# Kernel optimization log

Hardware: AMD Instinct MI355X
Metric: run time of the kernel (lower is better)

The kernel has to match this reference:

```python
import jax, jax.numpy as jnp
import numpy as np

N_NODES = 100000
N_EDGES = 3200000
N_GRAPHS = 512
IN_DIM = 29   # NUM_COMPONENT_TYPES(15) + NUM_PARAMS(14)
HID = 128
LAT = 256


def setup_inputs() -> dict:
    key = jax.random.key(0)
    ks = jax.random.split(key, 16)
    x = jax.random.normal(ks[0], (N_NODES, IN_DIM), dtype=jnp.float32)
    edge_index = jax.random.randint(ks[1], (2, N_EDGES), 0, N_NODES, dtype=jnp.int64)
    batch = jnp.sort(jax.random.randint(ks[2], (N_NODES,), 0, N_GRAPHS, dtype=jnp.int64))

    def lin(k, fan_in, fan_out):
        kw, kb = jax.random.split(k)
        s = 1.0 / np.sqrt(fan_in)
        W = jax.random.uniform(kw, (fan_in, fan_out), minval=-s, maxval=s, dtype=jnp.float32)
        b = jax.random.uniform(kb, (fan_out,), minval=-s, maxval=s, dtype=jnp.float32)
        return W, b

    W1, b1 = lin(ks[3], IN_DIM, HID)
    W2, b2 = lin(ks[4], HID, HID)
    W3, b3 = lin(ks[5], HID, HID)
    Wmu, bmu = lin(ks[6], HID, LAT)
    Wlv, blv = lin(ks[7], HID, LAT)
    return {"x": x, "edge_index": edge_index, "batch": batch,
            "W1": W1, "b1": b1, "W2": W2, "b2": b2, "W3": W3, "b3": b3,
            "Wmu": Wmu, "bmu": bmu, "Wlv": Wlv, "blv": blv}


def _gcn_conv(h, W, b, src, dst, dis):
    # PyG GCNConv: out = D^-1/2 (A + I) D^-1/2 (h W) + b
    hw = h @ W                                   # [N, out]
    norm = dis[src] * dis[dst]                   # [E]
    agg = jax.ops.segment_sum(hw[src] * norm[:, None], dst, num_segments=h.shape[0])
    return agg + hw * (dis * dis)[:, None] + b   # self-loop term has norm dis[i]^2


def reference(x, edge_index, batch, W1, b1, W2, b2, W3, b3, Wmu, bmu, Wlv, blv):
    src, dst = edge_index[0], edge_index[1]
    # symmetric degree with self-loops (computed once, identical across layers)
    deg = jax.ops.segment_sum(jnp.ones(src.shape[0], jnp.float32), dst,
                              num_segments=x.shape[0]) + 1.0
    dis = jax.lax.rsqrt(deg)

    h = jax.nn.relu(_gcn_conv(x, W1, b1, src, dst, dis))
    h = jax.nn.relu(_gcn_conv(h, W2, b2, src, dst, dis))
    h = jax.nn.relu(_gcn_conv(h, W3, b3, src, dst, dis))

    # global_mean_pool over graph ids
    sums = jax.ops.segment_sum(h, batch, num_segments=N_GRAPHS)
    cnts = jax.ops.segment_sum(jnp.ones(h.shape[0], jnp.float32), batch,
                               num_segments=N_GRAPHS)
    pooled = sums / jnp.maximum(cnts, 1.0)[:, None]   # [G, HID]

    mu = pooled @ Wmu + bmu
    logvar = pooled @ Wlv + blv
    return (mu, logvar)
```

## Files before the change

kernel.cpp:

```cpp
#include <hip/hip_runtime.h>
#include <hip/hip_bf16.h>

#define N_NODES 100000
#define N_EDGES 3200000
#define N_GRAPHS 512
#define IN_DIM 29
#define HID 128
#define LAT 256
#define NB 391
#define CAP 9216

typedef unsigned int uint;
typedef unsigned short ushort;
typedef float v4f __attribute__((ext_vector_type(4)));
typedef short v8s __attribute__((ext_vector_type(8)));

__device__ __forceinline__ ushort f2bf(float f) {
    uint u = __float_as_uint(f);
    return (ushort)((u + 0x7FFFu + ((u >> 16) & 1u)) >> 16);
}
__device__ __forceinline__ float bf2f(ushort h) { return __uint_as_float(((uint)h) << 16); }
__device__ __forceinline__ float bf_lo(uint p) { return __uint_as_float(p << 16); }
__device__ __forceinline__ float bf_hi(uint p) { return __uint_as_float(p & 0xFFFF0000u); }
__device__ __forceinline__ uint pack2(float a, float b) {
    return (uint)f2bf(a) | ((uint)f2bf(b) << 16);
}

__device__ __forceinline__ void bfadd(float* a, uint4 q) {
    a[0] += bf_lo(q.x); a[1] += bf_hi(q.x);
    a[2] += bf_lo(q.y); a[3] += bf_hi(q.y);
    a[4] += bf_lo(q.z); a[5] += bf_hi(q.z);
    a[6] += bf_lo(q.w); a[7] += bf_hi(q.w);
}


__global__ __launch_bounds__(1024, 2) void k_binA(const int* __restrict__ src, const int* __restrict__ dst,
                                                  int* __restrict__ bktCnt, int* __restrict__ packed, int e) {
    __shared__ int hist[NB];
    __shared__ int base[NB];
    int t = threadIdx.x;
    for (int i = t; i < NB; i += 1024) hist[i] = 0;
    __syncthreads();
    int d[8], s[8];
    const int blockStart = blockIdx.x * 8192;
    #pragma unroll
    for (int k = 0; k < 8; ++k) {
        int idx = blockStart + k * 1024 + t;
        if (idx < e) {
            d[k] = dst[idx];
            s[k] = src[idx];
            atomicAdd(&hist[d[k] >> 8], 1);
        } else d[k] = -1;
    }
    __syncthreads();
    for (int i = t; i < NB; i += 1024) {
        int c = hist[i];
        base[i] = c ? atomicAdd(&bktCnt[i], c) : 0;
    }
    __syncthreads();
    #pragma unroll
    for (int k = 0; k < 8; ++k) {
        if (d[k] >= 0) {
            int b = d[k] >> 8;
            int pos = atomicAdd(&base[b], 1);
            if (pos < CAP) packed[b * CAP + pos] = ((d[k] & 255) << 17) | s[k];
        }
    }
}

__global__ __launch_bounds__(512) void k_bscan(const int* __restrict__ bktCnt, int* __restrict__ colStart) {
    __shared__ int sh[512];
    int t = threadIdx.x;
    int v = (t < NB) ? bktCnt[t] : 0;
    if (v > CAP) v = CAP;
    sh[t] = v;
    __syncthreads();
    for (int off = 1; off < 512; off <<= 1) {
        int x = (t >= off) ? sh[t - off] : 0;
        __syncthreads();
        sh[t] += x;
        __syncthreads();
    }
    int excl = sh[t] - v;
    if (t <= NB) colStart[t] = excl;
}

__global__ __launch_bounds__(1024, 2) void k_binB(const int* __restrict__ bktCnt, const int* __restrict__ colStart,
                                                  const int* __restrict__ packed, int* __restrict__ col,
                                                  int* __restrict__ rp, float* __restrict__ dis,
                                                  const float* __restrict__ x, float* __restrict__ xt, int n) {
    __shared__ int cnt[8192];
    __shared__ int sh[1024];
    __shared__ float sdis[256];
    const int b = blockIdx.x;
    int cntB = bktCnt[b];
    if (cntB > CAP) cntB = CAP;
    const int segS = b * CAP;
    const int colBase = colStart[b];
    int t = threadIdx.x;
    #pragma unroll
    for (int k = 0; k < 8; ++k) cnt[t + k * 1024] = 0;
    __syncthreads();
    for (int j = t; j < cntB; j += 1024) {
        int pk = packed[segS + j];
        int key = ((pk >> 17) << 5) | ((pk & 0x1FFFF) >> 12);
        atomicAdd(&cnt[key], 1);
    }
    __syncthreads();
    int base8 = t << 3;
    int v[8];
    int sum = 0;
    #pragma unroll
    for (int k = 0; k < 8; ++k) { v[k] = cnt[base8 + k]; sum += v[k]; }
    sh[t] = sum;
    __syncthreads();
    for (int off = 1; off < 1024; off <<= 1) {
        int x2 = (t >= off) ? sh[t - off] : 0;
        __syncthreads();
        sh[t] += x2;
        __syncthreads();
    }
    int run = colBase + sh[t] - sum;
    #pragma unroll
    for (int k = 0; k < 8; ++k) { cnt[base8 + k] = run; run += v[k]; }
    __syncthreads();
    if (t < 256) {
        int node = (b << 8) + t;
        int start = cnt[t << 5];
        int next = (t == 255) ? (colBase + cntB) : cnt[(t + 1) << 5];
        int deg = next - start;
        float dv = rsqrtf((float)deg + 1.0f);
        sdis[t] = dv;
        if (node <= n) rp[node] = start;
        if (node < n) dis[node] = dv;
    }
    __syncthreads();
    for (int idx = t; idx < 256 * 32; idx += 1024) {
        int loc = idx >> 5;
        int node = (b << 8) + loc;
        if (node < n) {
            int k = idx & 31;
            float vv = (k < IN_DIM) ? x[(size_t)node * IN_DIM + k] * sdis[loc] : 0.f;
            xt[((size_t)node << 5) + k] = vv;
        }
    }
    for (int j = t; j < cntB; j += 1024) {
        int pk = packed[segS + j];
        int key = ((pk >> 17) << 5) | ((pk & 0x1FFFF) >> 12);
        int pos = atomicAdd(&cnt[key], 1);
        col[pos] = pk & 0x1FFFF;
    }
}


__device__ __forceinline__ void pack_one(const float* W, ushort* hi, ushort* lo, int Ksrc, int idx) {
    int j = idx & 7;
    int lane = (idx >> 3) & 63;
    int nt = (idx >> 9) & 7;
    int ks = idx >> 12;
    int k = ks * 32 + (lane >> 4) * 8 + j;
    int n = nt * 16 + (lane & 15);
    float v = (k < Ksrc) ? W[k * 128 + n] : 0.f;
    ushort h = f2bf(v);
    ushort l = f2bf(v - bf2f(h));
    hi[idx] = h;
    lo[idx] = l;
}

__global__ __launch_bounds__(256) void k_pack_all(const float* __restrict__ W1, const float* __restrict__ W2,
                                                  const float* __restrict__ W3,
                                                  ushort* w1h, ushort* w1l, ushort* w2h, ushort* w2l,
                                                  ushort* w3h, ushort* w3l, int* __restrict__ bktCnt) {
    int idx = blockIdx.x * 256 + threadIdx.x;
    if (idx < NB) bktCnt[idx] = 0;
    if (idx < 4096) {
        pack_one(W1, w1h, w1l, IN_DIM, idx);
    } else if (idx < 4096 + 16384) {
        pack_one(W2, w2h, w2l, HID, idx - 4096);
    } else if (idx < 4096 + 32768) {
        pack_one(W3, w3h, w3l, HID, idx - 4096 - 16384);
    }
}


__global__ __launch_bounds__(256, 6) void k_agg29(const float* __restrict__ xt, const int* __restrict__ rp,
                                                  const int* __restrict__ col, const float* __restrict__ dis,
                                                  float* __restrict__ y, int n) {
    int node = (int)((blockIdx.x * 256 + threadIdx.x) >> 3);
    if (node >= n) return;
    int c4 = (threadIdx.x & 7) << 2;
    int s = rp[node], e = rp[node + 1];
    v4f A = (v4f){0.f, 0.f, 0.f, 0.f};
    v4f B = (v4f){0.f, 0.f, 0.f, 0.f};
    int j = s;
    for (; j + 7 < e; j += 8) {
        int c0 = col[j],     c1 = col[j + 1], c2 = col[j + 2], c3 = col[j + 3];
        int c4i = col[j + 4], c5 = col[j + 5], c6 = col[j + 6], c7 = col[j + 7];
        v4f q0 = *(const v4f*)(xt + ((size_t)c0 << 5) + c4);
        v4f q1 = *(const v4f*)(xt + ((size_t)c1 << 5) + c4);
        v4f q2 = *(const v4f*)(xt + ((size_t)c2 << 5) + c4);
        v4f q3 = *(const v4f*)(xt + ((size_t)c3 << 5) + c4);
        v4f q4 = *(const v4f*)(xt + ((size_t)c4i << 5) + c4);
        v4f q5 = *(const v4f*)(xt + ((size_t)c5 << 5) + c4);
        v4f q6 = *(const v4f*)(xt + ((size_t)c6 << 5) + c4);
        v4f q7 = *(const v4f*)(xt + ((size_t)c7 << 5) + c4);
        A += q0; B += q1; A += q2; B += q3;
        A += q4; B += q5; A += q6; B += q7;
    }
    if (j + 3 < e) {
        int c0 = col[j], c1 = col[j + 1], c2 = col[j + 2], c3 = col[j + 3];
        v4f q0 = *(const v4f*)(xt + ((size_t)c0 << 5) + c4);
        v4f q1 = *(const v4f*)(xt + ((size_t)c1 << 5) + c4);
        v4f q2 = *(const v4f*)(xt + ((size_t)c2 << 5) + c4);
        v4f q3 = *(const v4f*)(xt + ((size_t)c3 << 5) + c4);
        A += q0; B += q1; A += q2; B += q3;
        j += 4;
    }
    for (; j < e; ++j) {
        int c = col[j];
        A += *(const v4f*)(xt + ((size_t)c << 5) + c4);
    }
    A += *(const v4f*)(xt + ((size_t)node << 5) + c4);
    float dv = dis[node];
    v4f o = (A + B) * dv;
    *(v4f*)(y + ((size_t)node << 5) + c4) = o;
}

__global__ __launch_bounds__(256, 6) void k_gemm1(const float* __restrict__ in,
                                                  const ushort* __restrict__ Whi,
                                                  const ushort* __restrict__ Wlo,
                                                  const float* __restrict__ bias,
                                                  ushort* __restrict__ out, int n) {
    const int wave = threadIdx.x >> 6;
    const int lane = threadIdx.x & 63;
    const int m0 = (blockIdx.x * 4 + wave) * 16;
    if (m0 >= n) return;
    int row = m0 + (lane & 15);
    if (row >= n) row = n - 1;
    const int kh = (lane >> 4) * 8;
    const float* rptr = in + ((size_t)row << 5) + kh;

    v4f acc[8];
    #pragma unroll
    for (int t = 0; t < 8; ++t) acc[t] = (v4f){0.f, 0.f, 0.f, 0.f};

    float a[8];
    #pragma unroll
    for (int j = 0; j < 8; ++j) a[j] = rptr[j];
    v8s ahi, alo;
    #pragma unroll
    for (int j = 0; j < 8; ++j) {
        ushort h = f2bf(a[j]);
        ushort l = f2bf(a[j] - bf2f(h));
        ahi[j] = (short)h;
        alo[j] = (short)l;
    }
    const ushort* bh = Whi + (size_t)lane * 8;
    const ushort* bl = Wlo + (size_t)lane * 8;
    #pragma unroll
    for (int nt = 0; nt < 8; ++nt) {
        v8s bhi = *(const v8s*)(bh + nt * 512);
        v8s blo = *(const v8s*)(bl + nt * 512);
        acc[nt] = __builtin_amdgcn_mfma_f32_16x16x32_bf16(ahi, bhi, acc[nt], 0, 0, 0);
        acc[nt] = __builtin_amdgcn_mfma_f32_16x16x32_bf16(ahi, blo, acc[nt], 0, 0, 0);
        acc[nt] = __builtin_amdgcn_mfma_f32_16x16x32_bf16(alo, bhi, acc[nt], 0, 0, 0);
    }

    const int orow0 = m0 + (lane >> 4) * 4;
    const int col0 = lane & 15;
    float bb[8];
    #pragma unroll
    for (int nt = 0; nt < 8; ++nt) bb[nt] = bias[nt * 16 + col0];
    #pragma unroll
    for (int r = 0; r < 4; ++r) {
        int orow = orow0 + r;
        if (orow < n) {
            #pragma unroll
            for (int nt = 0; nt < 8; ++nt)
                out[(size_t)orow * 128 + nt * 16 + col0] = f2bf(fmaxf(acc[nt][r] + bb[nt], 0.f));
        }
    }
}


__global__ __launch_bounds__(256, 4) void k_gemm_bf32(const ushort* __restrict__ in,
                                                      const ushort* __restrict__ Whi,
                                                      const ushort* __restrict__ Wlo,
                                                      const float* __restrict__ dis,
                                                      ushort* __restrict__ out, int n) {
    const int wave = threadIdx.x >> 6;
    const int lane = threadIdx.x & 63;
    const int m0 = (blockIdx.x * 4 + wave) * 32;
    if (m0 >= n) return;
    int row0 = m0 + (lane & 15);
    int row1 = row0 + 16;
    if (row0 >= n) row0 = n - 1;
    if (row1 >= n) row1 = n - 1;
    const int kh = (lane >> 4) * 8;
    const ushort* rp0 = in + (size_t)row0 * 128 + kh;
    const ushort* rp1 = in + (size_t)row1 * 128 + kh;

    v4f acc0[8], acc1[8];
    #pragma unroll
    for (int t = 0; t < 8; ++t) {
        acc0[t] = (v4f){0.f, 0.f, 0.f, 0.f};
        acc1[t] = (v4f){0.f, 0.f, 0.f, 0.f};
    }

    #pragma unroll
    for (int ks = 0; ks < 4; ++ks) {
        v8s a0 = *(const v8s*)(rp0 + ks * 32);
        v8s a1 = *(const v8s*)(rp1 + ks * 32);
        const ushort* bh = Whi + (size_t)(ks * 8) * 512 + (size_t)lane * 8;
        const ushort* bl = Wlo + (size_t)(ks * 8) * 512 + (size_t)lane * 8;
        #pragma unroll
        for (int nt = 0; nt < 8; ++nt) {
            v8s bhi = *(const v8s*)(bh + nt * 512);
            v8s blo = *(const v8s*)(bl + nt * 512);
            acc0[nt] = __builtin_amdgcn_mfma_f32_16x16x32_bf16(a0, bhi, acc0[nt], 0, 0, 0);
            acc0[nt] = __builtin_amdgcn_mfma_f32_16x16x32_bf16(a0, blo, acc0[nt], 0, 0, 0);
            acc1[nt] = __builtin_amdgcn_mfma_f32_16x16x32_bf16(a1, bhi, acc1[nt], 0, 0, 0);
            acc1[nt] = __builtin_amdgcn_mfma_f32_16x16x32_bf16(a1, blo, acc1[nt], 0, 0, 0);
        }
    }

    const int col0 = lane & 15;
    const int orow0 = m0 + (lane >> 4) * 4;
    #pragma unroll
    for (int r = 0; r < 4; ++r) {
        int orow = orow0 + r;
        if (orow < n) {
            float dv = dis[orow];
            #pragma unroll
            for (int nt = 0; nt < 8; ++nt)
                out[(size_t)orow * 128 + nt * 16 + col0] = f2bf(acc0[nt][r] * dv);
        }
        int orow2 = orow + 16;
        if (orow2 < n) {
            float dv = dis[orow2];
            #pragma unroll
            for (int nt = 0; nt < 8; ++nt)
                out[(size_t)orow2 * 128 + nt * 16 + col0] = f2bf(acc1[nt][r] * dv);
        }
    }
}


__global__ __launch_bounds__(256, 6) void k_agg(const ushort* __restrict__ hws, const int* __restrict__ rp,
                                                const int* __restrict__ col, const float* __restrict__ dis,
                                                const float* __restrict__ bias, ushort* __restrict__ out, int n) {
    int g = blockIdx.x * 32 + (threadIdx.x >> 3);
    int node = (g < n) ? g : g - n;
    if (g >= 2 * n) return;
    int c8 = ((g < n) ? 0 : 64) + ((threadIdx.x & 7) << 3);
    int s = rp[node], e = rp[node + 1];
    float A[8] = {0.f, 0.f, 0.f, 0.f, 0.f, 0.f, 0.f, 0.f};
    float B[8] = {0.f, 0.f, 0.f, 0.f, 0.f, 0.f, 0.f, 0.f};
    int j = s;
    for (; j + 7 < e; j += 8) {
        int c0 = col[j],     c1 = col[j + 1], c2 = col[j + 2], c3 = col[j + 3];
        int c4 = col[j + 4], c5 = col[j + 5], c6 = col[j + 6], c7 = col[j + 7];
        uint4 q0 = *(const uint4*)(hws + ((size_t)c0 << 7) + c8);
        uint4 q1 = *(const uint4*)(hws + ((size_t)c1 << 7) + c8);
        uint4 q2 = *(const uint4*)(hws + ((size_t)c2 << 7) + c8);
        uint4 q3 = *(const uint4*)(hws + ((size_t)c3 << 7) + c8);
        uint4 q4 = *(const uint4*)(hws + ((size_t)c4 << 7) + c8);
        uint4 q5 = *(const uint4*)(hws + ((size_t)c5 << 7) + c8);
        uint4 q6 = *(const uint4*)(hws + ((size_t)c6 << 7) + c8);
        uint4 q7 = *(const uint4*)(hws + ((size_t)c7 << 7) + c8);
        bfadd(A, q0); bfadd(B, q1); bfadd(A, q2); bfadd(B, q3);
        bfadd(A, q4); bfadd(B, q5); bfadd(A, q6); bfadd(B, q7);
    }
    if (j + 3 < e) {
        int c0 = col[j], c1 = col[j + 1], c2 = col[j + 2], c3 = col[j + 3];
        uint4 q0 = *(const uint4*)(hws + ((size_t)c0 << 7) + c8);
        uint4 q1 = *(const uint4*)(hws + ((size_t)c1 << 7) + c8);
        uint4 q2 = *(const uint4*)(hws + ((size_t)c2 << 7) + c8);
        uint4 q3 = *(const uint4*)(hws + ((size_t)c3 << 7) + c8);
        bfadd(A, q0); bfadd(B, q1); bfadd(A, q2); bfadd(B, q3);
        j += 4;
    }
    for (; j < e; ++j) {
        int c = col[j];
        uint4 q = *(const uint4*)(hws + ((size_t)c << 7) + c8);
        bfadd(A, q);
    }
    uint4 qs = *(const uint4*)(hws + ((size_t)node << 7) + c8);
    bfadd(A, qs);
    float dv = dis[node];
    float4 bv0 = *(const float4*)(bias + c8);
    float4 bv1 = *(const float4*)(bias + c8 + 4);
    float r0 = fmaxf(dv * (A[0] + B[0]) + bv0.x, 0.f);
    float r1 = fmaxf(dv * (A[1] + B[1]) + bv0.y, 0.f);
    float r2 = fmaxf(dv * (A[2] + B[2]) + bv0.z, 0.f);
    float r3 = fmaxf(dv * (A[3] + B[3]) + bv0.w, 0.f);
    float r4 = fmaxf(dv * (A[4] + B[4]) + bv1.x, 0.f);
    float r5 = fmaxf(dv * (A[5] + B[5]) + bv1.y, 0.f);
    float r6 = fmaxf(dv * (A[6] + B[6]) + bv1.z, 0.f);
    float r7 = fmaxf(dv * (A[7] + B[7]) + bv1.w, 0.f);
    uint4 o;
    o.x = pack2(r0, r1);
    o.y = pack2(r2, r3);
    o.z = pack2(r4, r5);
    o.w = pack2(r6, r7);
    *(uint4*)(out + (size_t)node * 128 + c8) = o;
}


__global__ __launch_bounds__(256) void k_pool_head(const ushort* __restrict__ h, const int* __restrict__ batch,
                                                   const float* __restrict__ Wmu, const float* __restrict__ bmu,
                                                   const float* __restrict__ Wlv, const float* __restrict__ blv,
                                                   float* __restrict__ out, int n) {
    int g = blockIdx.x;
    int t = threadIdx.x;
    int lo = 0, hi = n;
    while (lo < hi) { int m = (lo + hi) >> 1; if (batch[m] < g) lo = m + 1; else hi = m; }
    int start = lo;
    hi = n;
    while (lo < hi) { int m = (lo + hi) >> 1; if (batch[m] < g + 1) lo = m + 1; else hi = m; }
    int end = lo;

    __shared__ float sh0[256];
    __shared__ float sh1[256];
    __shared__ float pooled[128];
    int lane = t & 63;
    int grp = t >> 6;
    float a0 = 0.f, a1 = 0.f;
    for (int i = start + grp; i < end; i += 4) {
        uint q = *(const uint*)(h + (size_t)i * 128 + lane * 2);
        a0 += bf_lo(q);
        a1 += bf_hi(q);
    }
    sh0[t] = a0;
    sh1[t] = a1;
    __syncthreads();
    if (t < 64) {
        float cnt = (float)(end - start);
        float inv = 1.0f / fmaxf(cnt, 1.0f);
        float s0 = sh0[t] + sh0[t + 64] + sh0[t + 128] + sh0[t + 192];
        float s1 = sh1[t] + sh1[t + 64] + sh1[t + 128] + sh1[t + 192];
        pooled[t * 2] = s0 * inv;
        pooled[t * 2 + 1] = s1 * inv;
    }
    __syncthreads();
    float amu = bmu[t], alv = blv[t];
    for (int k = 0; k < 128; k += 4) {
        float p0 = pooled[k], p1 = pooled[k + 1], p2 = pooled[k + 2], p3 = pooled[k + 3];
        amu += p0 * Wmu[(k + 0) * 256 + t] + p1 * Wmu[(k + 1) * 256 + t]
             + p2 * Wmu[(k + 2) * 256 + t] + p3 * Wmu[(k + 3) * 256 + t];
        alv += p0 * Wlv[(k + 0) * 256 + t] + p1 * Wlv[(k + 1) * 256 + t]
             + p2 * Wlv[(k + 2) * 256 + t] + p3 * Wlv[(k + 3) * 256 + t];
    }
    out[(size_t)g * 256 + t] = amu;
    out[(size_t)N_GRAPHS * 256 + (size_t)g * 256 + t] = alv;
}


extern "C" void kernel_launch(void* const* d_in, const int* in_sizes, int n_in,
                              void* d_out, int out_size, void* d_ws, size_t ws_size,
                              hipStream_t stream) {
    const float* x    = (const float*)d_in[0];
    const int*   eidx = (const int*)d_in[1];
    const int*   batch= (const int*)d_in[2];
    const float* W1   = (const float*)d_in[3];
    const float* b1   = (const float*)d_in[4];
    const float* W2   = (const float*)d_in[5];
    const float* b2   = (const float*)d_in[6];
    const float* W3   = (const float*)d_in[7];
    const float* b3   = (const float*)d_in[8];
    const float* Wmu  = (const float*)d_in[9];
    const float* bmu  = (const float*)d_in[10];
    const float* Wlv  = (const float*)d_in[11];
    const float* blv  = (const float*)d_in[12];
    float* out = (float*)d_out;

    const int N = N_NODES, E = N_EDGES;
    const int* srcp = eidx;
    const int* dstp = eidx + E;

    ushort* w1h = (ushort*)d_ws;
    ushort* w1l = w1h + 4096;
    ushort* w2h = w1l + 4096;
    ushort* w2l = w2h + 16384;
    ushort* w3h = w2l + 16384;
    ushort* w3l = w3h + 16384;
    ushort* A   = w3l + 16384;
    ushort* B   = A + (size_t)N * 128;
    float*  dis = (float*)(B + (size_t)N * 128);
    int*   rp   = (int*)(dis + N);
    int*   bktCnt   = rp + (N + 2);
    int*   colStart = bktCnt + 512;
    int*   packed = colStart + 512;
    int*   col    = packed + (size_t)NB * CAP;

    float* xt = (float*)A;
    float* yv = xt + (size_t)N * 32;

    const int gE8192 = (E + 8191) / 8192;

    k_pack_all<<<144, 256, 0, stream>>>(W1, W2, W3, w1h, w1l, w2h, w2l, w3h, w3l, bktCnt);

    k_binA<<<gE8192, 1024, 0, stream>>>(srcp, dstp, bktCnt, packed, E);
    k_bscan<<<1, 512, 0, stream>>>(bktCnt, colStart);
    k_binB<<<NB, 1024, 0, stream>>>(bktCnt, colStart, packed, col, rp, dis, x, xt, N);

    const int gGemm1 = (N + 63) / 64;
    const int gGemm2 = (N + 127) / 128;
    const int gAgg29 = (N * 8 + 255) / 256;
    const int gAgg   = (2 * N + 31) / 32;

    k_agg29<<<gAgg29, 256, 0, stream>>>(xt, rp, col, dis, yv, N);
    k_gemm1<<<gGemm1, 256, 0, stream>>>(yv, w1h, w1l, b1, B, N);

    k_gemm_bf32<<<gGemm2, 256, 0, stream>>>(B, w2h, w2l, dis, A, N);
    k_agg<<<gAgg, 256, 0, stream>>>(A, rp, col, dis, b2, B, N);
    k_gemm_bf32<<<gGemm2, 256, 0, stream>>>(B, w3h, w3l, dis, A, N);
    k_agg<<<gAgg, 256, 0, stream>>>(A, rp, col, dis, b3, B, N);
    k_pool_head<<<N_GRAPHS, 256, 0, stream>>>(B, batch, Wmu, bmu, Wlv, blv, out, N);
}
```

Baseline: 473.2 us.

## Fuse layer-1 aggregation with GEMM and fold bucket scan into binB

The first-layer neighbour aggregation and its GEMM now run in one kernel. Each block aggregates 32 nodes into shared memory, then four waves run the MFMA split-bf16 GEMM on that tile, so the intermediate 32-float-per-node buffer never goes through global memory. The separate single-block bucket prefix scan is removed. Each binB block instead sums the preceding bucket counts with a shared-memory reduction, which saves two launches but repeats a small O(NB) amount of work in every block.

```diff
diff --git a/kernel.cpp b/kernel.cpp
--- a/kernel.cpp
+++ b/kernel.cpp
@@ -68,24 +68,7 @@
     }
 }
 
-__global__ __launch_bounds__(512) void k_bscan(const int* __restrict__ bktCnt, int* __restrict__ colStart) {
-    __shared__ int sh[512];
-    int t = threadIdx.x;
-    int v = (t < NB) ? bktCnt[t] : 0;
-    if (v > CAP) v = CAP;
-    sh[t] = v;
-    __syncthreads();
-    for (int off = 1; off < 512; off <<= 1) {
-        int x = (t >= off) ? sh[t - off] : 0;
-        __syncthreads();
-        sh[t] += x;
-        __syncthreads();
-    }
-    int excl = sh[t] - v;
-    if (t <= NB) colStart[t] = excl;
-}
-
-__global__ __launch_bounds__(1024, 2) void k_binB(const int* __restrict__ bktCnt, const int* __restrict__ colStart,
+__global__ __launch_bounds__(1024, 2) void k_binB(const int* __restrict__ bktCnt,
                                                   const int* __restrict__ packed, int* __restrict__ col,
                                                   int* __restrict__ rp, float* __restrict__ dis,
                                                   const float* __restrict__ x, float* __restrict__ xt, int n) {
@@ -96,11 +79,21 @@
     int cntB = bktCnt[b];
     if (cntB > CAP) cntB = CAP;
     const int segS = b * CAP;
-    const int colBase = colStart[b];
     int t = threadIdx.x;
+    int part = 0;
+    for (int i = t; i < b; i += 1024) {
+        int c = bktCnt[i];
+        part += (c > CAP) ? CAP : c;
+    }
     #pragma unroll
     for (int k = 0; k < 8; ++k) cnt[t + k * 1024] = 0;
-    __syncthreads();
+    sh[t] = part;
+    __syncthreads();
+    for (int off = 512; off > 0; off >>= 1) {
+        if (t < off) sh[t] += sh[t + off];
+        __syncthreads();
+    }
+    const int colBase = sh[0];
     for (int j = t; j < cntB; j += 1024) {
         int pk = packed[segS + j];
         int key = ((pk >> 17) << 5) | ((pk & 0x1FFFF) >> 12);
@@ -183,70 +176,64 @@
 }
 
 
-__global__ __launch_bounds__(256, 6) void k_agg29(const float* __restrict__ xt, const int* __restrict__ rp,
-                                                  const int* __restrict__ col, const float* __restrict__ dis,
-                                                  float* __restrict__ y, int n) {
-    int node = (int)((blockIdx.x * 256 + threadIdx.x) >> 3);
-    if (node >= n) return;
-    int c4 = (threadIdx.x & 7) << 2;
-    int s = rp[node], e = rp[node + 1];
-    v4f A = (v4f){0.f, 0.f, 0.f, 0.f};
-    v4f B = (v4f){0.f, 0.f, 0.f, 0.f};
-    int j = s;
-    for (; j + 7 < e; j += 8) {
-        int c0 = col[j],     c1 = col[j + 1], c2 = col[j + 2], c3 = col[j + 3];
-        int c4i = col[j + 4], c5 = col[j + 5], c6 = col[j + 6], c7 = col[j + 7];
-        v4f q0 = *(const v4f*)(xt + ((size_t)c0 << 5) + c4);
-        v4f q1 = *(const v4f*)(xt + ((size_t)c1 << 5) + c4);
-        v4f q2 = *(const v4f*)(xt + ((size_t)c2 << 5) + c4);
-        v4f q3 = *(const v4f*)(xt + ((size_t)c3 << 5) + c4);
-        v4f q4 = *(const v4f*)(xt + ((size_t)c4i << 5) + c4);
-        v4f q5 = *(const v4f*)(xt + ((size_t)c5 << 5) + c4);
-        v4f q6 = *(const v4f*)(xt + ((size_t)c6 << 5) + c4);
-        v4f q7 = *(const v4f*)(xt + ((size_t)c7 << 5) + c4);
-        A += q0; B += q1; A += q2; B += q3;
-        A += q4; B += q5; A += q6; B += q7;
-    }
-    if (j + 3 < e) {
-        int c0 = col[j], c1 = col[j + 1], c2 = col[j + 2], c3 = col[j + 3];
-        v4f q0 = *(const v4f*)(xt + ((size_t)c0 << 5) + c4);
-        v4f q1 = *(const v4f*)(xt + ((size_t)c1 << 5) + c4);
-        v4f q2 = *(const v4f*)(xt + ((size_t)c2 << 5) + c4);
-        v4f q3 = *(const v4f*)(xt + ((size_t)c3 << 5) + c4);
-        A += q0; B += q1; A += q2; B += q3;
-        j += 4;
-    }
-    for (; j < e; ++j) {
-        int c = col[j];
-        A += *(const v4f*)(xt + ((size_t)c << 5) + c4);
-    }
-    A += *(const v4f*)(xt + ((size_t)node << 5) + c4);
-    float dv = dis[node];
-    v4f o = (A + B) * dv;
-    *(v4f*)(y + ((size_t)node << 5) + c4) = o;
-}
-
-__global__ __launch_bounds__(256, 6) void k_gemm1(const float* __restrict__ in,
-                                                  const ushort* __restrict__ Whi,
-                                                  const ushort* __restrict__ Wlo,
-                                                  const float* __restrict__ bias,
-                                                  ushort* __restrict__ out, int n) {
-    const int wave = threadIdx.x >> 6;
-    const int lane = threadIdx.x & 63;
-    const int m0 = (blockIdx.x * 4 + wave) * 16;
-    if (m0 >= n) return;
-    int row = m0 + (lane & 15);
-    if (row >= n) row = n - 1;
+__global__ __launch_bounds__(256, 6) void k_l1(const float* __restrict__ xt, const int* __restrict__ rp,
+                                               const int* __restrict__ col, const float* __restrict__ dis,
+                                               const ushort* __restrict__ Whi, const ushort* __restrict__ Wlo,
+                                               const float* __restrict__ bias, ushort* __restrict__ out, int n) {
+    __shared__ float yl[32][36];
+    int t = threadIdx.x;
+    int loc = t >> 3;
+    int node = blockIdx.x * 32 + loc;
+    int c4 = (t & 7) << 2;
+    if (node < n) {
+        int s = rp[node], e = rp[node + 1];
+        v4f A = (v4f){0.f, 0.f, 0.f, 0.f};
+        v4f B = (v4f){0.f, 0.f, 0.f, 0.f};
+        int j = s;
+        for (; j + 7 < e; j += 8) {
+            int c0 = col[j],     c1 = col[j + 1], c2 = col[j + 2], c3 = col[j + 3];
+            int c4i = col[j + 4], c5 = col[j + 5], c6 = col[j + 6], c7 = col[j + 7];
+            v4f q0 = *(const v4f*)(xt + ((size_t)c0 << 5) + c4);
+            v4f q1 = *(const v4f*)(xt + ((size_t)c1 << 5) + c4);
+            v4f q2 = *(const v4f*)(xt + ((size_t)c2 << 5) + c4);
+            v4f q3 = *(const v4f*)(xt + ((size_t)c3 << 5) + c4);
+            v4f q4 = *(const v4f*)(xt + ((size_t)c4i << 5) + c4);
+            v4f q5 = *(const v4f*)(xt + ((size_t)c5 << 5) + c4);
+            v4f q6 = *(const v4f*)(xt + ((size_t)c6 << 5) + c4);
+            v4f q7 = *(const v4f*)(xt + ((size_t)c7 << 5) + c4);
+            A += q0; B += q1; A += q2; B += q3;
+            A += q4; B += q5; A += q6; B += q7;
+        }
+        if (j + 3 < e) {
+            int c0 = col[j], c1 = col[j + 1], c2 = col[j + 2], c3 = col[j + 3];
+            v4f q0 = *(const v4f*)(xt + ((size_t)c0 << 5) + c4);
+            v4f q1 = *(const v4f*)(xt + ((size_t)c1 << 5) + c4);
+            v4f q2 = *(const v4f*)(xt + ((size_t)c2 << 5) + c4);
+            v4f q3 = *(const v4f*)(xt + ((size_t)c3 << 5) + c4);
+            A += q0; B += q1; A += q2; B += q3;
+            j += 4;
+        }
+        for (; j < e; ++j) {
+            int c = col[j];
+            A += *(const v4f*)(xt + ((size_t)c << 5) + c4);
+        }
+        A += *(const v4f*)(xt + ((size_t)node << 5) + c4);
+        float dv = dis[node];
+        v4f o = (A + B) * dv;
+        yl[loc][c4 + 0] = o.x;
+        yl[loc][c4 + 1] = o.y;
+        yl[loc][c4 + 2] = o.z;
+        yl[loc][c4 + 3] = o.w;
+    }
+    __syncthreads();
+    const int wave = t >> 6;
+    const int lane = t & 63;
+    const int mrow = ((wave >> 1) << 4) + (lane & 15);
+    const int ntBase = (wave & 1) * 4;
     const int kh = (lane >> 4) * 8;
-    const float* rptr = in + ((size_t)row << 5) + kh;
-
-    v4f acc[8];
-    #pragma unroll
-    for (int t = 0; t < 8; ++t) acc[t] = (v4f){0.f, 0.f, 0.f, 0.f};
-
     float a[8];
     #pragma unroll
-    for (int j = 0; j < 8; ++j) a[j] = rptr[j];
+    for (int j = 0; j < 8; ++j) a[j] = yl[mrow][kh + j];
     v8s ahi, alo;
     #pragma unroll
     for (int j = 0; j < 8; ++j) {
@@ -257,27 +244,30 @@
     }
     const ushort* bh = Whi + (size_t)lane * 8;
     const ushort* bl = Wlo + (size_t)lane * 8;
-    #pragma unroll
-    for (int nt = 0; nt < 8; ++nt) {
+    v4f acc[4];
+    #pragma unroll
+    for (int i = 0; i < 4; ++i) acc[i] = (v4f){0.f, 0.f, 0.f, 0.f};
+    #pragma unroll
+    for (int i = 0; i < 4; ++i) {
+        int nt = ntBase + i;
         v8s bhi = *(const v8s*)(bh + nt * 512);
         v8s blo = *(const v8s*)(bl + nt * 512);
-        acc[nt] = __builtin_amdgcn_mfma_f32_16x16x32_bf16(ahi, bhi, acc[nt], 0, 0, 0);
-        acc[nt] = __builtin_amdgcn_mfma_f32_16x16x32_bf16(ahi, blo, acc[nt], 0, 0, 0);
-        acc[nt] = __builtin_amdgcn_mfma_f32_16x16x32_bf16(alo, bhi, acc[nt], 0, 0, 0);
-    }
-
-    const int orow0 = m0 + (lane >> 4) * 4;
+        acc[i] = __builtin_amdgcn_mfma_f32_16x16x32_bf16(ahi, bhi, acc[i], 0, 0, 0);
+        acc[i] = __builtin_amdgcn_mfma_f32_16x16x32_bf16(ahi, blo, acc[i], 0, 0, 0);
+        acc[i] = __builtin_amdgcn_mfma_f32_16x16x32_bf16(alo, bhi, acc[i], 0, 0, 0);
+    }
     const int col0 = lane & 15;
-    float bb[8];
-    #pragma unroll
-    for (int nt = 0; nt < 8; ++nt) bb[nt] = bias[nt * 16 + col0];
+    const int orow0 = blockIdx.x * 32 + ((wave >> 1) << 4) + ((lane >> 4) << 2);
+    float bb[4];
+    #pragma unroll
+    for (int i = 0; i < 4; ++i) bb[i] = bias[(ntBase + i) * 16 + col0];
     #pragma unroll
     for (int r = 0; r < 4; ++r) {
         int orow = orow0 + r;
         if (orow < n) {
             #pragma unroll
-            for (int nt = 0; nt < 8; ++nt)
-                out[(size_t)orow * 128 + nt * 16 + col0] = f2bf(fmaxf(acc[nt][r] + bb[nt], 0.f));
+            for (int i = 0; i < 4; ++i)
+                out[(size_t)orow * 128 + (ntBase + i) * 16 + col0] = f2bf(fmaxf(acc[i][r] + bb[i], 0.f));
         }
     }
 }
@@ -494,23 +484,19 @@
     int*   col    = packed + (size_t)NB * CAP;
 
     float* xt = (float*)A;
-    float* yv = xt + (size_t)N * 32;
 
     const int gE8192 = (E + 8191) / 8192;
 
     k_pack_all<<<144, 256, 0, stream>>>(W1, W2, W3, w1h, w1l, w2h, w2l, w3h, w3l, bktCnt);
 
     k_binA<<<gE8192, 1024, 0, stream>>>(srcp, dstp, bktCnt, packed, E);
-    k_bscan<<<1, 512, 0, stream>>>(bktCnt, colStart);
-    k_binB<<<NB, 1024, 0, stream>>>(bktCnt, colStart, packed, col, rp, dis, x, xt, N);
-
-    const int gGemm1 = (N + 63) / 64;
+    k_binB<<<NB, 1024, 0, stream>>>(bktCnt, packed, col, rp, dis, x, xt, N);
+
     const int gGemm2 = (N + 127) / 128;
-    const int gAgg29 = (N * 8 + 255) / 256;
+    const int gL1    = (N + 31) / 32;
     const int gAgg   = (2 * N + 31) / 32;
 
-    k_agg29<<<gAgg29, 256, 0, stream>>>(xt, rp, col, dis, yv, N);
-    k_gemm1<<<gGemm1, 256, 0, stream>>>(yv, w1h, w1l, b1, B, N);
+    k_l1<<<gL1, 256, 0, stream>>>(xt, rp, col, dis, w1h, w1l, b1, B, N);
 
     k_gemm_bf32<<<gGemm2, 256, 0, stream>>>(B, w2h, w2l, dis, A, N);
     k_agg<<<gAgg, 256, 0, stream>>>(A, rp, col, dis, b2, B, N);
```

Result: faster. 457.8 us (-3.3%).
